# Optimization experiments

Hardware: AMD Instinct MI355X
Metric: run time of the kernel (lower is better)

## Reference

```python
import jax, jax.numpy as jnp
import numpy as np

B, S, D = 4, 2048, 768
H, DH = 12, 64  # num heads, head dim


def setup_inputs() -> dict:
    key = jax.random.key(0)
    ks = jax.random.split(key, 4)
    scale = 0.02
    return {
        "hidden_states": jax.random.normal(ks[0], (B, S, D), dtype=jnp.float32),
        "attention_mask": jnp.zeros((B, 1, 1, S), dtype=jnp.float32),
        "Wq": jax.random.normal(ks[1], (D, D), dtype=jnp.float32) * scale,
        "bq": jnp.zeros((D,), dtype=jnp.float32),
        "Wk": jax.random.normal(ks[2], (D, D), dtype=jnp.float32) * scale,
        "bk": jnp.zeros((D,), dtype=jnp.float32),
        "Wv": jax.random.normal(ks[3], (D, D), dtype=jnp.float32) * scale,
        "bv": jnp.zeros((D,), dtype=jnp.float32),
    }


def _split_heads(x):
    # [B, S, D] -> [B, H, S, DH]
    b, s, _ = x.shape
    return x.reshape(b, s, H, DH).transpose(0, 2, 1, 3)


def reference(hidden_states, attention_mask, Wq, bq, Wk, bk, Wv, bv):
    q = _split_heads(hidden_states @ Wq.T + bq)
    k = _split_heads(hidden_states @ Wk.T + bk)
    v = _split_heads(hidden_states @ Wv.T + bv)
    # scores: [B, H, S, S]
    scores = jnp.einsum("bhqd,bhkd->bhqk", q, k) / jnp.sqrt(jnp.float32(DH))
    scores = scores + attention_mask
    probs = jax.nn.softmax(scores, axis=-1)
    # dropout prob = 0.0 (eval) -> identity
    ctx = jnp.einsum("bhqk,bhkd->bhqd", probs, v)
    ctx = ctx.transpose(0, 2, 1, 3).reshape(hidden_states.shape[0], hidden_states.shape[1], D)
    return ctx
```

## Files before the change

kernel.cpp:

```cpp
#include <hip/hip_runtime.h>

#define S_LEN 2048
#define DMODEL 768
#define NH 12
#define DHEAD 64
#define BATCH 4
#define MROWS (BATCH * S_LEN)
#define NQKV 2304
#define LOG2E 1.4426950408889634f

using short8 = __attribute__((ext_vector_type(8))) short;
using f32x4  = __attribute__((ext_vector_type(4))) float;
using f32x16 = __attribute__((ext_vector_type(16))) float;

typedef const __attribute__((address_space(1))) void* gas_ptr;
typedef __attribute__((address_space(3))) void* las_ptr;

__device__ __forceinline__ void gl2lds16(const void* g, void* l) {
  __builtin_amdgcn_global_load_lds((gas_ptr)(unsigned long long)g,
                                   (las_ptr)(unsigned int)(unsigned long long)l,
                                   16, 0, 0);
}

__device__ __forceinline__ float fexp2(float x) {
  float r;
  asm("v_exp_f32 %0, %1" : "=v"(r) : "v"(x));
  return r;
}

__device__ __forceinline__ unsigned cvtpk(float lo, float hi) {
  unsigned r;
  asm("v_cvt_pk_bf16_f32 %0, %1, %2" : "=v"(r) : "v"(lo), "v"(hi));
  return r;
}

__device__ __forceinline__ void plswap(unsigned &a, unsigned &b) {
  asm("v_permlane32_swap_b32 %0, %1" : "+v"(a), "+v"(b));
}

__global__ __launch_bounds__(256) void prep_kernel(
    const float* __restrict__ hs, const float* __restrict__ Wq,
    const float* __restrict__ Wk, const float* __restrict__ Wv,
    const float* __restrict__ mask,
    unsigned short* __restrict__ Xb, unsigned short* __restrict__ Wall,
    float* __restrict__ mask2)
{
  const int NX = MROWS * DMODEL / 4;
  const int NW = DMODEL * DMODEL / 4;
  const int NM = (BATCH * S_LEN) / 4;
  int i = blockIdx.x * 256 + threadIdx.x;
  if (i < NX) {
    float4 f = ((const float4*)hs)[i];
    uint2 o = { cvtpk(f.x, f.y), cvtpk(f.z, f.w) };
    ((uint2*)Xb)[i] = o;
  } else if (i < NX + 3 * NW) {
    int j = i - NX;
    int sec = j / NW, r = j - sec * NW;
    const float* src = (sec == 0) ? Wq : (sec == 1) ? Wk : Wv;
    float4 f = ((const float4*)src)[r];
    uint2 o = { cvtpk(f.x, f.y), cvtpk(f.z, f.w) };
    ((uint2*)(Wall + (size_t)sec * DMODEL * DMODEL))[r] = o;
  } else if (i < NX + 3 * NW + NM) {
    int r = i - NX - 3 * NW;
    float4 m = ((const float4*)mask)[r];
    float4 o = { (m.x - 10.f) * LOG2E, (m.y - 10.f) * LOG2E,
                 (m.z - 10.f) * LOG2E, (m.w - 10.f) * LOG2E };
    ((float4*)mask2)[r] = o;
  }
}

__global__ __launch_bounds__(256) void qkv_gemm(
    const unsigned short* __restrict__ Xb,
    const unsigned short* __restrict__ Wall,
    const float* __restrict__ bq,
    const float* __restrict__ bk,
    const float* __restrict__ bv,
    unsigned short* __restrict__ Out)
{
  __shared__ __align__(16) short As[128][64];
  __shared__ __align__(16) short Bs[128][64];

  int m0 = blockIdx.y * 128;
  int n0 = blockIdx.x * 128;
  int t = threadIdx.x;
  int w = t >> 6, lane = t & 63, lg = lane >> 4, lc = lane & 15;
  int wr = (w >> 1) * 64, wc = (w & 1) * 64;

  int srow = lane >> 3;
  int schunk = (lane & 7) ^ srow;

  f32x4 acc[4][4] = {};

  for (int k0 = 0; k0 < DMODEL; k0 += 64) {
    __syncthreads();
    for (int it = 0; it < 4; ++it) {
      int rb = w * 32 + it * 8;
      int r = rb + srow;
      gl2lds16(&Xb[(size_t)(m0 + r) * DMODEL + k0 + schunk * 8], &As[rb][0]);
      gl2lds16(&Wall[(size_t)(n0 + r) * DMODEL + k0 + schunk * 8], &Bs[rb][0]);
    }
    __syncthreads();
    for (int ks = 0; ks < 2; ++ks) {
      short8 a[4], b[4];
      for (int mt = 0; mt < 4; ++mt)
        a[mt] = *(const short8*)&As[wr + mt * 16 + lc][(((ks * 4 + lg) ^ (lc & 7))) * 8];
      for (int nt = 0; nt < 4; ++nt)
        b[nt] = *(const short8*)&Bs[wc + nt * 16 + lc][(((ks * 4 + lg) ^ (lc & 7))) * 8];
      for (int mt = 0; mt < 4; ++mt)
        for (int nt = 0; nt < 4; ++nt)
          acc[mt][nt] = __builtin_amdgcn_mfma_f32_16x16x32_bf16(a[mt], b[nt], acc[mt][nt], 0, 0, 0);
    }
  }

  for (int nt = 0; nt < 4; ++nt) {
    int col = n0 + wc + nt * 16 + lc;
    float bb = (col < 768) ? bq[col] : (col < 1536) ? bk[col - 768] : bv[col - 1536];
    float sc = (col < 768) ? (0.125f * LOG2E) : 1.0f;
    for (int mt = 0; mt < 4; ++mt) {
      int row = m0 + wr + mt * 16 + lg * 4;
      for (int i = 0; i < 4; ++i) {
        float v = (acc[mt][nt][i] + bb) * sc;
        Out[(size_t)(row + i) * NQKV + col] = (unsigned short)cvtpk(v, v);
      }
    }
  }
}

__global__ __launch_bounds__(256) void v_transpose(
    const unsigned short* __restrict__ QKV,
    unsigned short* __restrict__ Vt)
{
  int st = blockIdx.x, h = blockIdx.y, b = blockIdx.z;
  __shared__ __align__(16) short Ls[64][72];
  int t = threadIdx.x;
  int s0 = st * 64;
  int lr = t >> 3, ls = (t & 7) * 8;
  for (int it = 0; it < 2; ++it) {
    int r = lr + it * 32;
    *(int4*)&Ls[r][ls] =
        *(const int4*)&QKV[(size_t)(b * S_LEN + s0 + r) * NQKV + 1536 + h * DHEAD + ls];
  }
  __syncthreads();
  int d = t & 63, sq = t >> 6;
  size_t obase = ((size_t)((b * NH + h) * DHEAD + d)) * S_LEN + s0;
  for (int it = 0; it < 2; ++it) {
    int ss = sq + it * 4;
    short8 vv;
    for (int j = 0; j < 8; ++j) vv[j] = Ls[ss * 8 + j][d];
    *(short8*)&Vt[obase + ss * 8] = vv;
  }
}

__global__ __launch_bounds__(256, 4) void flash_attn(
    const unsigned short* __restrict__ QKV,
    const unsigned short* __restrict__ Vt,
    const float* __restrict__ mask2,
    float* __restrict__ out)
{
  int qt = blockIdx.x, h = blockIdx.y, b = blockIdx.z;
  __shared__ __align__(16) short Ks[2][64][64];
  __shared__ __align__(16) short Vts[2][64][64];

  int t = threadIdx.x, w = t >> 6, lane = t & 63;
  int m31 = lane & 31, hf = lane >> 5;
  int q0 = qt * 128;
  int srow = lane >> 3;
  int schunk = (lane & 7) ^ srow;

  short8 qf[4];
  {
    size_t qrow = (size_t)(b * S_LEN + q0 + w * 32 + m31) * NQKV + h * DHEAD;
#pragma unroll
    for (int kk = 0; kk < 4; ++kk)
      qf[kk] = *(const short8*)&QKV[qrow + kk * 16 + hf * 8];
  }

  float lsum = 0.f;
  f32x16 o[2] = {};
  size_t vtbase = (size_t)((b * NH + h) * DHEAD) * S_LEN;
  size_t kbase0 = (size_t)(b * S_LEN) * NQKV + 768 + h * DHEAD;
  const float* mrow = mask2 + (size_t)b * S_LEN;

#pragma unroll
  for (int it = 0; it < 2; ++it) {
    int rb = w * 16 + it * 8;
    int r = rb + srow;
    gl2lds16(&QKV[kbase0 + (size_t)r * NQKV + schunk * 8], &Ks[0][rb][0]);
    gl2lds16(&Vt[vtbase + (size_t)r * S_LEN + schunk * 8], &Vts[0][rb][0]);
  }

  int buf = 0;
  for (int kt = 0; kt < S_LEN / 64; ++kt) {
    int k0 = kt * 64;
    __syncthreads();

    {
      int ktn = (kt + 1 < S_LEN / 64) ? (kt + 1) : kt;
      int k0n = ktn * 64;
#pragma unroll
      for (int it = 0; it < 2; ++it) {
        int rb = w * 16 + it * 8;
        int r = rb + srow;
        gl2lds16(&QKV[kbase0 + (size_t)(k0n + r) * NQKV + schunk * 8], &Ks[buf ^ 1][rb][0]);
        gl2lds16(&Vt[vtbase + (size_t)r * S_LEN + k0n + schunk * 8], &Vts[buf ^ 1][rb][0]);
      }
    }

    f32x16 s[2] = {};
    __builtin_amdgcn_s_setprio(1);
#pragma unroll
    for (int kk = 0; kk < 4; ++kk)
#pragma unroll
      for (int mt = 0; mt < 2; ++mt) {
        int r = mt * 32 + m31;
        short8 ak = *(const short8*)&Ks[buf][r][((kk * 2 + hf) ^ (r & 7)) * 8];
        s[mt] = __builtin_amdgcn_mfma_f32_32x32x16_bf16(ak, qf[kk], s[mt], 0, 0, 0);
      }
    __builtin_amdgcn_s_setprio(0);

    unsigned pw[2][4][2];
#pragma unroll
    for (int mt = 0; mt < 2; ++mt)
#pragma unroll
      for (int g = 0; g < 4; ++g) {
        float4 mv = *(const float4*)&mrow[k0 + mt * 32 + g * 8 + hf * 4];
        float p0 = fexp2(s[mt][g * 4 + 0] + mv.x);
        float p1 = fexp2(s[mt][g * 4 + 1] + mv.y);
        float p2 = fexp2(s[mt][g * 4 + 2] + mv.z);
        float p3 = fexp2(s[mt][g * 4 + 3] + mv.w);
        lsum += (p0 + p1) + (p2 + p3);
        pw[mt][g][0] = cvtpk(p0, p1);
        pw[mt][g][1] = cvtpk(p2, p3);
      }

#pragma unroll
    for (int mt = 0; mt < 2; ++mt)
#pragma unroll
      for (int kk2 = 0; kk2 < 2; ++kk2) {
        unsigned a0 = pw[mt][2 * kk2][0], b0 = pw[mt][2 * kk2 + 1][0];
        unsigned a1 = pw[mt][2 * kk2][1], b1 = pw[mt][2 * kk2 + 1][1];
        plswap(a0, b0);
        plswap(a1, b1);
        union { unsigned u[4]; short8 v; } fr;
        fr.u[0] = a0; fr.u[1] = a1; fr.u[2] = b0; fr.u[3] = b1;
        int kk = mt * 2 + kk2;
        __builtin_amdgcn_s_setprio(1);
#pragma unroll
        for (int nt = 0; nt < 2; ++nt) {
          int r = nt * 32 + m31;
          short8 bvv = *(const short8*)&Vts[buf][r][((kk * 2 + hf) ^ (r & 7)) * 8];
          o[nt] = __builtin_amdgcn_mfma_f32_32x32x16_bf16(fr.v, bvv, o[nt], 0, 0, 0);
        }
        __builtin_amdgcn_s_setprio(0);
      }

    buf ^= 1;
  }

  lsum += __shfl_xor(lsum, 32, 64);
  float inv = 1.0f / lsum;
  float lv[16];
#pragma unroll
  for (int r = 0; r < 16; ++r)
    lv[r] = __shfl(inv, (r & 3) + 8 * (r >> 2) + 4 * hf, 64);

  for (int nt = 0; nt < 2; ++nt)
    for (int r = 0; r < 16; ++r) {
      int qrow = (r & 3) + 8 * (r >> 2) + 4 * hf;
      int q = q0 + w * 32 + qrow;
      out[(size_t)(b * S_LEN + q) * DMODEL + h * DHEAD + nt * 32 + m31] = o[nt][r] * lv[r];
    }
}

extern "C" void kernel_launch(void* const* d_in, const int* in_sizes, int n_in,
                              void* d_out, int out_size, void* d_ws, size_t ws_size,
                              hipStream_t stream) {
  const float* hs   = (const float*)d_in[0];
  const float* mask = (const float*)d_in[1];
  const float* Wq   = (const float*)d_in[2];
  const float* bq   = (const float*)d_in[3];
  const float* Wk   = (const float*)d_in[4];
  const float* bk   = (const float*)d_in[5];
  const float* Wv   = (const float*)d_in[6];
  const float* bv   = (const float*)d_in[7];
  float* out = (float*)d_out;

  char* ws = (char*)d_ws;
  const size_t XB_BYTES   = (size_t)MROWS * DMODEL * 2;
  const size_t QKV_BYTES  = (size_t)MROWS * NQKV * 2;
  const size_t WALL_BYTES = (size_t)NQKV * DMODEL * 2;
  unsigned short* Xb    = (unsigned short*)ws;
  unsigned short* QKV   = (unsigned short*)(ws + XB_BYTES);
  unsigned short* Wall  = (unsigned short*)(ws + XB_BYTES + QKV_BYTES);
  float*          mask2 = (float*)(ws + XB_BYTES + QKV_BYTES + WALL_BYTES);
  unsigned short* Vtg   = Xb;

  const int NX = MROWS * DMODEL / 4;
  const int NW = DMODEL * DMODEL / 4;
  const int NM = (BATCH * S_LEN) / 4;
  int nprep = NX + 3 * NW + NM;
  prep_kernel<<<(nprep + 255) / 256, 256, 0, stream>>>(hs, Wq, Wk, Wv, mask, Xb, Wall, mask2);

  qkv_gemm<<<dim3(NQKV / 128, MROWS / 128), 256, 0, stream>>>(Xb, Wall, bq, bk, bv, QKV);

  v_transpose<<<dim3(S_LEN / 64, NH, BATCH), 256, 0, stream>>>(QKV, Vtg);

  flash_attn<<<dim3(S_LEN / 128, NH, BATCH), 256, 0, stream>>>(QKV, Vtg, mask2, out);
}
```

Baseline: 232.0 us.

## Hand-schedule flash attention loop with explicit LDS reads, waitcnts, and staged mask

Reworks the attention inner loop into a manually unrolled two-buffer step. K and V fragments are read from LDS with inline ds_read_b128 and explicit s_waitcnt/sched_barrier, so the LDS reads overlap the MFMAs. The mask row is staged once into shared memory instead of being read from global memory each tile, and the sum accumulator is split in two. Occupancy hint drops from 4 to 3 blocks per CU because of the extra LDS and registers. Manual waitcnt counts risk being wrong if the compiler reorders or inserts memory ops.

```diff
diff --git a/kernel.cpp b/kernel.cpp
--- a/kernel.cpp
+++ b/kernel.cpp
@@ -37,6 +37,19 @@
 __device__ __forceinline__ void plswap(unsigned &a, unsigned &b) {
   asm("v_permlane32_swap_b32 %0, %1" : "+v"(a), "+v"(b));
 }
+
+__device__ __forceinline__ short8 lds_read_s8(unsigned a) {
+  short8 r; asm volatile("ds_read_b128 %0, %1" : "=v"(r) : "v"(a)); return r;
+}
+__device__ __forceinline__ f32x4 lds_read_f4(unsigned a) {
+  f32x4 r; asm volatile("ds_read_b128 %0, %1" : "=v"(r) : "v"(a)); return r;
+}
+__device__ __forceinline__ unsigned lofs(const void* p) {
+  return (unsigned)(unsigned long long)p;
+}
+
+#define SWAIT(cnt) do { asm volatile("s_waitcnt " cnt); \
+  __builtin_amdgcn_sched_barrier(0); } while (0)
 
 __global__ __launch_bounds__(256) void prep_kernel(
     const float* __restrict__ hs, const float* __restrict__ Wq,
@@ -151,15 +164,16 @@
   }
 }
 
-__global__ __launch_bounds__(256, 4) void flash_attn(
+__global__ __launch_bounds__(256, 3) void flash_attn(
     const unsigned short* __restrict__ QKV,
     const unsigned short* __restrict__ Vt,
     const float* __restrict__ mask2,
     float* __restrict__ out)
 {
   int qt = blockIdx.x, h = blockIdx.y, b = blockIdx.z;
-  __shared__ __align__(16) short Ks[2][64][64];
-  __shared__ __align__(16) short Vts[2][64][64];
+  __shared__ __align__(16) short Ks0[64][64], Ks1[64][64];
+  __shared__ __align__(16) short Vts0[64][64], Vts1[64][64];
+  __shared__ __align__(16) float Ms[S_LEN];
 
   int t = threadIdx.x, w = t >> 6, lane = t & 63;
   int m31 = lane & 31, hf = lane >> 5;
@@ -167,6 +181,10 @@
   int srow = lane >> 3;
   int schunk = (lane & 7) ^ srow;
 
+  size_t vtbase = (size_t)((b * NH + h) * DHEAD) * S_LEN;
+  size_t kbase0 = (size_t)(b * S_LEN) * NQKV + 768 + h * DHEAD;
+  const float* mrow = mask2 + (size_t)b * S_LEN;
+
   short8 qf[4];
   {
     size_t qrow = (size_t)(b * S_LEN + q0 + w * 32 + m31) * NQKV + h * DHEAD;
@@ -175,64 +193,101 @@
       qf[kk] = *(const short8*)&QKV[qrow + kk * 16 + hf * 8];
   }
 
-  float lsum = 0.f;
-  f32x16 o[2] = {};
-  size_t vtbase = (size_t)((b * NH + h) * DHEAD) * S_LEN;
-  size_t kbase0 = (size_t)(b * S_LEN) * NQKV + 768 + h * DHEAD;
-  const float* mrow = mask2 + (size_t)b * S_LEN;
-
+#pragma unroll
+  for (int it = 0; it < 2; ++it) {
+    int c = w * 2 + it;
+    gl2lds16(&mrow[c * 256 + lane * 4], &Ms[c * 256]);
+  }
 #pragma unroll
   for (int it = 0; it < 2; ++it) {
     int rb = w * 16 + it * 8;
     int r = rb + srow;
-    gl2lds16(&QKV[kbase0 + (size_t)r * NQKV + schunk * 8], &Ks[0][rb][0]);
-    gl2lds16(&Vt[vtbase + (size_t)r * S_LEN + schunk * 8], &Vts[0][rb][0]);
-  }
-
-  int buf = 0;
-  for (int kt = 0; kt < S_LEN / 64; ++kt) {
+    gl2lds16(&QKV[kbase0 + (size_t)r * NQKV + schunk * 8], &Ks0[rb][0]);
+    gl2lds16(&Vt[vtbase + (size_t)r * S_LEN + schunk * 8], &Vts0[rb][0]);
+  }
+  SWAIT("vmcnt(0)");
+  __builtin_amdgcn_s_barrier();
+  __builtin_amdgcn_sched_barrier(0);
+#pragma unroll
+  for (int kk = 0; kk < 4; ++kk) asm volatile("" :: "v"(qf[kk]));
+
+  float lsumA = 0.f, lsumB = 0.f;
+  f32x16 o[2] = {};
+  const f32x16 Zv = {};
+
+  auto step = [&](auto& KC, auto& VC, auto& KN, auto& VN, int kt) {
     int k0 = kt * 64;
-    __syncthreads();
+    SWAIT("vmcnt(0)");
+    __builtin_amdgcn_s_barrier();
+    __builtin_amdgcn_sched_barrier(0);
 
     {
-      int ktn = (kt + 1 < S_LEN / 64) ? (kt + 1) : kt;
+      int ktn = (kt + 1 < S_LEN / 64) ? kt + 1 : kt;
       int k0n = ktn * 64;
 #pragma unroll
       for (int it = 0; it < 2; ++it) {
         int rb = w * 16 + it * 8;
         int r = rb + srow;
-        gl2lds16(&QKV[kbase0 + (size_t)(k0n + r) * NQKV + schunk * 8], &Ks[buf ^ 1][rb][0]);
-        gl2lds16(&Vt[vtbase + (size_t)r * S_LEN + k0n + schunk * 8], &Vts[buf ^ 1][rb][0]);
+        gl2lds16(&QKV[kbase0 + (size_t)(k0n + r) * NQKV + schunk * 8], &KN[rb][0]);
+        gl2lds16(&Vt[vtbase + (size_t)r * S_LEN + k0n + schunk * 8], &VN[rb][0]);
       }
     }
 
-    f32x16 s[2] = {};
+    short8 ak[8];
+#pragma unroll
+    for (int kk = 0; kk < 4; ++kk)
+#pragma unroll
+      for (int mt = 0; mt < 2; ++mt)
+        ak[kk * 2 + mt] =
+            lds_read_s8(lofs(&KC[mt * 32 + m31][((kk * 2 + hf) ^ (m31 & 7)) * 8]));
+    f32x4 mre[8];
+#pragma unroll
+    for (int mt = 0; mt < 2; ++mt)
+#pragma unroll
+      for (int g = 0; g < 4; ++g)
+        mre[mt * 4 + g] = lds_read_f4(lofs(&Ms[k0 + mt * 32 + g * 8 + hf * 4]));
+
+    SWAIT("lgkmcnt(8)");
+
     __builtin_amdgcn_s_setprio(1);
+    f32x16 s0v = __builtin_amdgcn_mfma_f32_32x32x16_bf16(ak[0], qf[0], Zv, 0, 0, 0);
+    f32x16 s1v = __builtin_amdgcn_mfma_f32_32x32x16_bf16(ak[1], qf[0], Zv, 0, 0, 0);
+#pragma unroll
+    for (int kk = 1; kk < 4; ++kk) {
+      s0v = __builtin_amdgcn_mfma_f32_32x32x16_bf16(ak[kk * 2 + 0], qf[kk], s0v, 0, 0, 0);
+      s1v = __builtin_amdgcn_mfma_f32_32x32x16_bf16(ak[kk * 2 + 1], qf[kk], s1v, 0, 0, 0);
+    }
+    __builtin_amdgcn_s_setprio(0);
+
+    short8 vb[8];
 #pragma unroll
     for (int kk = 0; kk < 4; ++kk)
 #pragma unroll
-      for (int mt = 0; mt < 2; ++mt) {
-        int r = mt * 32 + m31;
-        short8 ak = *(const short8*)&Ks[buf][r][((kk * 2 + hf) ^ (r & 7)) * 8];
-        s[mt] = __builtin_amdgcn_mfma_f32_32x32x16_bf16(ak, qf[kk], s[mt], 0, 0, 0);
-      }
-    __builtin_amdgcn_s_setprio(0);
+      for (int nt = 0; nt < 2; ++nt)
+        vb[kk * 2 + nt] =
+            lds_read_s8(lofs(&VC[nt * 32 + m31][((kk * 2 + hf) ^ (m31 & 7)) * 8]));
+
+    SWAIT("lgkmcnt(8)");
 
     unsigned pw[2][4][2];
 #pragma unroll
-    for (int mt = 0; mt < 2; ++mt)
+    for (int mt = 0; mt < 2; ++mt) {
+      const f32x16& sv = mt ? s1v : s0v;
 #pragma unroll
       for (int g = 0; g < 4; ++g) {
-        float4 mv = *(const float4*)&mrow[k0 + mt * 32 + g * 8 + hf * 4];
-        float p0 = fexp2(s[mt][g * 4 + 0] + mv.x);
-        float p1 = fexp2(s[mt][g * 4 + 1] + mv.y);
-        float p2 = fexp2(s[mt][g * 4 + 2] + mv.z);
-        float p3 = fexp2(s[mt][g * 4 + 3] + mv.w);
-        lsum += (p0 + p1) + (p2 + p3);
+        f32x4 mv = mre[mt * 4 + g];
+        float p0 = fexp2(sv[g * 4 + 0] + mv[0]);
+        float p1 = fexp2(sv[g * 4 + 1] + mv[1]);
+        float p2 = fexp2(sv[g * 4 + 2] + mv[2]);
+        float p3 = fexp2(sv[g * 4 + 3] + mv[3]);
+        lsumA += p0 + p1;
+        lsumB += p2 + p3;
         pw[mt][g][0] = cvtpk(p0, p1);
         pw[mt][g][1] = cvtpk(p2, p3);
       }
-
+    }
+
+    short8 fr[4];
 #pragma unroll
     for (int mt = 0; mt < 2; ++mt)
 #pragma unroll
@@ -241,22 +296,29 @@
         unsigned a1 = pw[mt][2 * kk2][1], b1 = pw[mt][2 * kk2 + 1][1];
         plswap(a0, b0);
         plswap(a1, b1);
-        union { unsigned u[4]; short8 v; } fr;
-        fr.u[0] = a0; fr.u[1] = a1; fr.u[2] = b0; fr.u[3] = b1;
-        int kk = mt * 2 + kk2;
-        __builtin_amdgcn_s_setprio(1);
-#pragma unroll
-        for (int nt = 0; nt < 2; ++nt) {
-          int r = nt * 32 + m31;
-          short8 bvv = *(const short8*)&Vts[buf][r][((kk * 2 + hf) ^ (r & 7)) * 8];
-          o[nt] = __builtin_amdgcn_mfma_f32_32x32x16_bf16(fr.v, bvv, o[nt], 0, 0, 0);
-        }
-        __builtin_amdgcn_s_setprio(0);
+        union { unsigned u[4]; short8 v; } u_;
+        u_.u[0] = a0; u_.u[1] = a1; u_.u[2] = b0; u_.u[3] = b1;
+        fr[mt * 2 + kk2] = u_.v;
       }
 
-    buf ^= 1;
-  }
-
+    SWAIT("lgkmcnt(0)");
+
+    __builtin_amdgcn_s_setprio(1);
+#pragma unroll
+    for (int kk = 0; kk < 4; ++kk) {
+      o[0] = __builtin_amdgcn_mfma_f32_32x32x16_bf16(fr[kk], vb[kk * 2 + 0], o[0], 0, 0, 0);
+      o[1] = __builtin_amdgcn_mfma_f32_32x32x16_bf16(fr[kk], vb[kk * 2 + 1], o[1], 0, 0, 0);
+    }
+    __builtin_amdgcn_s_setprio(0);
+  };
+
+#pragma unroll 1
+  for (int i2 = 0; i2 < S_LEN / 128; ++i2) {
+    step(Ks0, Vts0, Ks1, Vts1, 2 * i2);
+    step(Ks1, Vts1, Ks0, Vts0, 2 * i2 + 1);
+  }
+
+  float lsum = lsumA + lsumB;
   lsum += __shfl_xor(lsum, 32, 64);
   float inv = 1.0f / lsum;
   float lv[16];
```

Result: slower. 410.5 us (+77.0%).

## Remap GEMM and attention blocks for XCD-aware L2 locality, hoist mask loads

Applied to the files above, without the earlier changes.

Both qkv_gemm and flash_attn switch to a 1D grid and remap block IDs so that blocks sharing operands (the same M rows in the GEMM, the same batch/head K/V in attention) land on the same XCD (gid & 7). This aims to raise L2 hit rates on the chiplet-partitioned MI355X. The attention loop also issues the mask loads at the top of each iteration behind scheduling barriers and disables unrolling of the key loop, so mask latency overlaps the prefetch and the QK MFMAs. The fixed barriers constrain the compiler's instruction scheduling, and the mask values held in registers across the QK MFMAs raise register pressure.

```diff
diff --git a/kernel.cpp b/kernel.cpp
--- a/kernel.cpp
+++ b/kernel.cpp
@@ -80,8 +80,14 @@
   __shared__ __align__(16) short As[128][64];
   __shared__ __align__(16) short Bs[128][64];
 
-  int m0 = blockIdx.y * 128;
-  int n0 = blockIdx.x * 128;
+  int gid = blockIdx.x;
+  int x = gid & 7;
+  int j = gid >> 3;
+  int mloc = j / 18;
+  int ntile = j - mloc * 18;
+  int m0 = (x * 8 + mloc) * 128;
+  int n0 = ntile * 128;
+
   int t = threadIdx.x;
   int w = t >> 6, lane = t & 63, lg = lane >> 4, lc = lane & 15;
   int wr = (w >> 1) * 64, wc = (w & 1) * 64;
@@ -157,7 +163,15 @@
     const float* __restrict__ mask2,
     float* __restrict__ out)
 {
-  int qt = blockIdx.x, h = blockIdx.y, b = blockIdx.z;
+  int gid = blockIdx.x;
+  int x = gid & 7;
+  int j = gid >> 3;
+  int gloc = j >> 4;
+  int qt = j & 15;
+  int g = gloc * 8 + x;
+  int h = g % NH;
+  int b = g / NH;
+
   __shared__ __align__(16) short Ks[2][64][64];
   __shared__ __align__(16) short Vts[2][64][64];
 
@@ -167,6 +181,10 @@
   int srow = lane >> 3;
   int schunk = (lane & 7) ^ srow;
 
+  size_t vtbase = (size_t)((b * NH + h) * DHEAD) * S_LEN;
+  size_t kbase0 = (size_t)(b * S_LEN) * NQKV + 768 + h * DHEAD;
+  const float* mrow = mask2 + (size_t)b * S_LEN;
+
   short8 qf[4];
   {
     size_t qrow = (size_t)(b * S_LEN + q0 + w * 32 + m31) * NQKV + h * DHEAD;
@@ -177,9 +195,6 @@
 
   float lsum = 0.f;
   f32x16 o[2] = {};
-  size_t vtbase = (size_t)((b * NH + h) * DHEAD) * S_LEN;
-  size_t kbase0 = (size_t)(b * S_LEN) * NQKV + 768 + h * DHEAD;
-  const float* mrow = mask2 + (size_t)b * S_LEN;
 
 #pragma unroll
   for (int it = 0; it < 2; ++it) {
@@ -190,9 +205,18 @@
   }
 
   int buf = 0;
+#pragma unroll 1
   for (int kt = 0; kt < S_LEN / 64; ++kt) {
     int k0 = kt * 64;
     __syncthreads();
+
+    f32x4 mv_[8];
+#pragma unroll
+    for (int mt = 0; mt < 2; ++mt)
+#pragma unroll
+      for (int gg = 0; gg < 4; ++gg)
+        mv_[mt * 4 + gg] = *(const f32x4*)&mrow[k0 + mt * 32 + gg * 8 + hf * 4];
+    __builtin_amdgcn_sched_barrier(0);
 
     {
       int ktn = (kt + 1 < S_LEN / 64) ? (kt + 1) : kt;
@@ -205,6 +229,7 @@
         gl2lds16(&Vt[vtbase + (size_t)r * S_LEN + k0n + schunk * 8], &Vts[buf ^ 1][rb][0]);
       }
     }
+    __builtin_amdgcn_sched_barrier(0);
 
     f32x16 s[2] = {};
     __builtin_amdgcn_s_setprio(1);
@@ -222,15 +247,15 @@
 #pragma unroll
     for (int mt = 0; mt < 2; ++mt)
 #pragma unroll
-      for (int g = 0; g < 4; ++g) {
-        float4 mv = *(const float4*)&mrow[k0 + mt * 32 + g * 8 + hf * 4];
-        float p0 = fexp2(s[mt][g * 4 + 0] + mv.x);
-        float p1 = fexp2(s[mt][g * 4 + 1] + mv.y);
-        float p2 = fexp2(s[mt][g * 4 + 2] + mv.z);
-        float p3 = fexp2(s[mt][g * 4 + 3] + mv.w);
+      for (int gg = 0; gg < 4; ++gg) {
+        f32x4 m4 = mv_[mt * 4 + gg];
+        float p0 = fexp2(s[mt][gg * 4 + 0] + m4[0]);
+        float p1 = fexp2(s[mt][gg * 4 + 1] + m4[1]);
+        float p2 = fexp2(s[mt][gg * 4 + 2] + m4[2]);
+        float p3 = fexp2(s[mt][gg * 4 + 3] + m4[3]);
         lsum += (p0 + p1) + (p2 + p3);
-        pw[mt][g][0] = cvtpk(p0, p1);
-        pw[mt][g][1] = cvtpk(p2, p3);
+        pw[mt][gg][0] = cvtpk(p0, p1);
+        pw[mt][gg][1] = cvtpk(p2, p3);
       }
 
 #pragma unroll
@@ -301,9 +326,9 @@
   int nprep = NX + 3 * NW + NM;
   prep_kernel<<<(nprep + 255) / 256, 256, 0, stream>>>(hs, Wq, Wk, Wv, mask, Xb, Wall, mask2);
 
-  qkv_gemm<<<dim3(NQKV / 128, MROWS / 128), 256, 0, stream>>>(Xb, Wall, bq, bk, bv, QKV);
+  qkv_gemm<<<1152, 256, 0, stream>>>(Xb, Wall, bq, bk, bv, QKV);
 
   v_transpose<<<dim3(S_LEN / 64, NH, BATCH), 256, 0, stream>>>(QKV, Vtg);
 
-  flash_attn<<<dim3(S_LEN / 128, NH, BATCH), 256, 0, stream>>>(QKV, Vtg, mask2, out);
-}
+  flash_attn<<<768, 256, 0, stream>>>(QKV, Vtg, mask2, out);
+}
```

After: 252.1 us. 8.7% more time.
